# Optimization experiments

Hardware: AMD Instinct MI355X
Metric: run time of the kernel (lower is better)

## Reference

```python
import jax, jax.numpy as jnp
import numpy as np

N, L, D = 8192, 50, 64          # batch nodes, history length, embed_dim
NUM_ITEMS, NUM_ATTRS, NUM_FAM = 50000, 100000, 100000


def setup_inputs() -> dict:
    key = jax.random.key(0)
    ks = jax.random.split(key, 12)
    scale = 0.05
    return {
        "nodes": jax.random.randint(ks[0], (N,), 0, NUM_ITEMS),
        "history_va": jax.random.randint(ks[1], (N, L), 0, NUM_ATTRS),
        "history_af": jax.random.randint(ks[2], (N, L), 0, NUM_FAM),
        "v2e_w": jax.random.normal(ks[3], (NUM_ITEMS, D), jnp.float32) * scale,
        "a2e_w": jax.random.normal(ks[4], (NUM_ATTRS, D), jnp.float32) * scale,
        "f2e_w": jax.random.normal(ks[5], (NUM_FAM, D), jnp.float32) * scale,
        "W1": jax.random.normal(ks[6], (3 * D, D), jnp.float32) * scale,
        "b1": jnp.zeros((D,), jnp.float32),
        "W2": jax.random.normal(ks[7], (D, D), jnp.float32) * scale,
        "b2": jnp.zeros((D,), jnp.float32),
        "w3": jax.random.normal(ks[8], (D, 1), jnp.float32) * scale,
        "b3": jnp.zeros((1,), jnp.float32),
    }


def reference(nodes, history_va, history_af, v2e_w, a2e_w, f2e_w,
              W1, b1, W2, b2, w3, b3):
    # Batched form of the per-node loop (va=True branch).
    e_va = a2e_w[history_va]                       # [N, L, D] gathered attr embeds
    e_af = f2e_w[history_af]                       # [N, L, D] gathered famous embeds
    va_rep = v2e_w[nodes]                          # [N, D]    target item embed
    rep = jnp.broadcast_to(va_rep[:, None, :], e_va.shape)
    x = jnp.concatenate([e_va, rep, e_af], axis=-1)  # [N, L, 3D]
    h = jax.nn.relu(x @ W1 + b1)                   # [N, L, D]
    h = jax.nn.relu(h @ W2 + b2)                   # [N, L, D]
    scores = (h @ w3 + b3)[..., 0]                 # [N, L]
    att = jax.nn.softmax(scores, axis=1)           # softmax over history dim
    # e_va.T @ att per node  ==  weighted sum over history
    return jnp.einsum("nld,nl->nd", e_va, att)     # [N, D]
```

## Files before the change

kernel.cpp:

```cpp
#include <hip/hip_runtime.h>
#include <hip/hip_bf16.h>

typedef __bf16    bf16x8 __attribute__((ext_vector_type(8)));
typedef __bf16    bf16x4 __attribute__((ext_vector_type(4)));
typedef _Float16  f16x8  __attribute__((ext_vector_type(8)));
typedef _Float16  f16x4  __attribute__((ext_vector_type(4)));
typedef float     f32x4  __attribute__((ext_vector_type(4)));

#define HL 50
#define DD 64


__global__ __launch_bounds__(256, 4) void prep_all_kernel(
    const int*   __restrict__ nodes,
    const float* __restrict__ v2e,
    const float* __restrict__ W1,
    const float* __restrict__ b1,
    const float* __restrict__ W2,
    const float* __restrict__ b2,
    const float* __restrict__ w3,
    _Float16* __restrict__ ba16,
    _Float16* __restrict__ wf, float* __restrict__ wsc,
    int N, int GB)
{
    __shared__ __align__(16) _Float16 es[64 * 72];
    const int tid  = threadIdx.x;
    const int w    = tid >> 6, lane = tid & 63;
    const int lq   = lane & 15, quad = lane >> 4;
    const int bid  = blockIdx.x;

    if (bid < GB) {
        const int col = w * 16 + lq;
        const int n0 = bid * 64;
        #pragma unroll
        for (int i = 0; i < 4; ++i) {
            int t = i * 256 + tid;
            int row = t >> 4, q = t & 15;
            int gn = n0 + row; if (gn >= N) gn = N - 1;
            int idx = nodes[gn];
            float4 v = *(const float4*)(v2e + (size_t)idx * DD + q * 4);
            f16x4 pk = {(_Float16)v.x, (_Float16)v.y, (_Float16)v.z, (_Float16)v.w};
            *(f16x4*)&es[row * 72 + q * 4] = pk;
        }
        f16x8 bfr[2];
        #pragma unroll
        for (int t = 0; t < 2; ++t)
            #pragma unroll
            for (int j = 0; j < 8; ++j)
                bfr[t][j] = (_Float16)W1[(64 + t * 32 + quad * 8 + j) * DD + col];
        const float b1c = b1[col];
        __syncthreads();

        f32x4 acc[4];
        #pragma unroll
        for (int mt = 0; mt < 4; ++mt) acc[mt] = (f32x4){0.f, 0.f, 0.f, 0.f};
        #pragma unroll
        for (int t = 0; t < 2; ++t)
            #pragma unroll
            for (int mt = 0; mt < 4; ++mt) {
                f16x8 a = *(const f16x8*)&es[(mt * 16 + lq) * 72 + t * 32 + quad * 8];
                acc[mt] = __builtin_amdgcn_mfma_f32_16x16x32_f16(a, bfr[t], acc[mt], 0, 0, 0);
            }
        #pragma unroll
        for (int mt = 0; mt < 4; ++mt)
            #pragma unroll
            for (int r = 0; r < 4; ++r) {
                int gn = n0 + mt * 16 + quad * 4 + r;
                if (gn < N) ba16[(size_t)gn * DD + col] = (_Float16)(acc[mt][r] + b1c);
            }
    } else {
        const int ln = tid & 63, c0 = tid >> 6;
        #pragma unroll
        for (int h = 0; h < 6; ++h) {
            int c = c0 + 4 * h;
            int part = c >> 3, cc = c & 7;
            int ct = cc >> 1, t = cc & 1;
            const float* S = (part == 2) ? W2 : W1;
            int koff = (part == 1) ? 128 : 0;
            _Float16* d = wf + ((size_t)c * 64 + ln) * 8;
            #pragma unroll
            for (int j = 0; j < 8; ++j)
                d[j] = (_Float16)S[(koff + t * 32 + (ln >> 4) * 8 + j) * DD
                                   + ct * 16 + (ln & 15)];
        }
        if (tid < 64) { wsc[tid] = w3[tid]; wsc[64 + tid] = b2[tid]; }
    }
}

__global__ __launch_bounds__(256, 2) void va_main_kernel(
    const int*      __restrict__ hva,
    const int*      __restrict__ haf,
    const float*    __restrict__ a2e,
    const float*    __restrict__ f2e,
    const _Float16* __restrict__ ba16,
    const _Float16* __restrict__ wf,
    const float*    __restrict__ wsc,
    float*          __restrict__ out, int Ntot)
{
    __shared__ __align__(16) _Float16 hs[4][64 * 72];
    const int tid  = threadIdx.x;
    const int w    = tid >> 6;
    const int lane = tid & 63;
    const int lq   = lane & 15;
    const int quad = lane >> 4;
    const int node = blockIdx.x * 4 + w;
    if (node >= Ntot) return;
    _Float16* ws_ = hs[w];

    const int* hb = hva + node * HL;
    const int* fb = haf + node * HL;
    const int lclamp = (lane < HL) ? lane : 0;
    const int iv  = hb[lclamp];
    const int ifv = fb[lclamp];

    float4 ra[4][2][2];
    #pragma unroll
    for (int mt = 0; mt < 4; ++mt) {
        const int row = mt * 16 + lq;
        const int ia  = __shfl(iv, row);
        #pragma unroll
        for (int t = 0; t < 2; ++t) {
            const float* p = a2e + (size_t)ia * DD + t * 32 + quad * 8;
            ra[mt][t][0] = *(const float4*)p;
            ra[mt][t][1] = *(const float4*)(p + 4);
        }
    }
    f16x8 xa[4][2];
    #pragma unroll
    for (int mt = 0; mt < 4; ++mt)
        #pragma unroll
        for (int t = 0; t < 2; ++t) {
            float4 v0 = ra[mt][t][0], v1 = ra[mt][t][1];
            xa[mt][t] = (f16x8){(_Float16)v0.x, (_Float16)v0.y, (_Float16)v0.z, (_Float16)v0.w,
                                (_Float16)v1.x, (_Float16)v1.y, (_Float16)v1.z, (_Float16)v1.w};
        }

    float4 rf[4][2][2];
    #pragma unroll
    for (int mt = 0; mt < 4; ++mt) {
        const int row = mt * 16 + lq;
        const int ifm = __shfl(ifv, row);
        #pragma unroll
        for (int t = 0; t < 2; ++t) {
            const float* p = f2e + (size_t)ifm * DD + t * 32 + quad * 8;
            rf[mt][t][0] = *(const float4*)p;
            rf[mt][t][1] = *(const float4*)(p + 4);
        }
    }

    f32x4 acc[4][4];
    #pragma unroll
    for (int ct = 0; ct < 4; ++ct) {
        const float bav = (float)ba16[(size_t)node * DD + ct * 16 + lq];
        #pragma unroll
        for (int mt = 0; mt < 4; ++mt)
            acc[mt][ct] = (f32x4){bav, bav, bav, bav};
    }
    #pragma unroll
    for (int ct = 0; ct < 4; ++ct)
        #pragma unroll
        for (int t = 0; t < 2; ++t) {
            f16x8 bfr = *(const f16x8*)(wf + ((size_t)(ct * 2 + t) * 64 + lane) * 8);
            #pragma unroll
            for (int mt = 0; mt < 4; ++mt)
                acc[mt][ct] = __builtin_amdgcn_mfma_f32_16x16x32_f16(xa[mt][t], bfr, acc[mt][ct], 0, 0, 0);
        }
    f16x8 xf[4][2];
    #pragma unroll
    for (int mt = 0; mt < 4; ++mt)
        #pragma unroll
        for (int t = 0; t < 2; ++t) {
            float4 v0 = rf[mt][t][0], v1 = rf[mt][t][1];
            xf[mt][t] = (f16x8){(_Float16)v0.x, (_Float16)v0.y, (_Float16)v0.z, (_Float16)v0.w,
                                (_Float16)v1.x, (_Float16)v1.y, (_Float16)v1.z, (_Float16)v1.w};
        }
    #pragma unroll
    for (int ct = 0; ct < 4; ++ct)
        #pragma unroll
        for (int t = 0; t < 2; ++t) {
            f16x8 bfr = *(const f16x8*)(wf + ((size_t)(8 + ct * 2 + t) * 64 + lane) * 8);
            #pragma unroll
            for (int mt = 0; mt < 4; ++mt)
                acc[mt][ct] = __builtin_amdgcn_mfma_f32_16x16x32_f16(xf[mt][t], bfr, acc[mt][ct], 0, 0, 0);
        }

    #pragma unroll
    for (int mt = 0; mt < 4; ++mt)
        #pragma unroll
        for (int ct = 0; ct < 4; ++ct)
            #pragma unroll
            for (int r = 0; r < 4; ++r) {
                const int row = mt * 16 + quad * 4 + r;
                float hv = (row < HL) ? fmaxf(acc[mt][ct][r], 0.f) : 0.f;
                ws_[row * 72 + ct * 16 + lq] = (_Float16)hv;
            }

    f16x8 h1f[4][2];
    #pragma unroll
    for (int mt = 0; mt < 4; ++mt)
        #pragma unroll
        for (int t = 0; t < 2; ++t)
            h1f[mt][t] = *(const f16x8*)&ws_[(mt * 16 + lq) * 72 + t * 32 + quad * 8];

    float sc[4][4];
    #pragma unroll
    for (int mt = 0; mt < 4; ++mt)
        #pragma unroll
        for (int r = 0; r < 4; ++r) sc[mt][r] = 0.f;

    #pragma unroll
    for (int ct = 0; ct < 4; ++ct) {
        const float b2c = wsc[64 + ct * 16 + lq];
        const float w3c = wsc[ct * 16 + lq];
        f16x8 bfr[2];
        #pragma unroll
        for (int t = 0; t < 2; ++t)
            bfr[t] = *(const f16x8*)(wf + ((size_t)(16 + ct * 2 + t) * 64 + lane) * 8);
        #pragma unroll
        for (int mt = 0; mt < 4; ++mt) {
            f32x4 a2 = {b2c, b2c, b2c, b2c};
            #pragma unroll
            for (int t = 0; t < 2; ++t)
                a2 = __builtin_amdgcn_mfma_f32_16x16x32_f16(h1f[mt][t], bfr[t], a2, 0, 0, 0);
            #pragma unroll
            for (int r = 0; r < 4; ++r)
                sc[mt][r] = fmaf(fmaxf(a2[r], 0.f), w3c, sc[mt][r]);
        }
    }

    #pragma unroll
    for (int mt = 0; mt < 4; ++mt)
        #pragma unroll
        for (int r = 0; r < 4; ++r)
            #pragma unroll
            for (int m = 1; m < 16; m <<= 1)
                sc[mt][r] += __shfl_xor(sc[mt][r], m);

    #pragma unroll
    for (int r = 0; r < 4; ++r)
        if (48 + quad * 4 + r >= HL) sc[3][r] = -3.0e38f;

    float mx = sc[0][0];
    #pragma unroll
    for (int mt = 0; mt < 4; ++mt)
        #pragma unroll
        for (int r = 0; r < 4; ++r) mx = fmaxf(mx, sc[mt][r]);
    mx = fmaxf(mx, __shfl_xor(mx, 16));
    mx = fmaxf(mx, __shfl_xor(mx, 32));

    float sm = 0.f;
    #pragma unroll
    for (int mt = 0; mt < 4; ++mt)
        #pragma unroll
        for (int r = 0; r < 4; ++r) {
            sc[mt][r] = __expf(sc[mt][r] - mx);
            sm += sc[mt][r];
        }
    sm += __shfl_xor(sm, 16);
    sm += __shfl_xor(sm, 32);
    const float inv = 1.f / sm;

    float oa[4] = {0.f, 0.f, 0.f, 0.f};
    #pragma unroll
    for (int l = 0; l < HL; ++l) {
        const int   srcl = ((l >> 2) & 3) << 4;
        const float av   = __shfl(sc[l >> 4][l & 3], srcl);
        const int   idx  = __builtin_amdgcn_readlane(iv, l);
        oa[l & 3] = fmaf(av, a2e[(size_t)idx * DD + lane], oa[l & 3]);
    }
    out[(size_t)node * DD + lane] = ((oa[0] + oa[1]) + (oa[2] + oa[3])) * inv;
}

#define FMR  112
#define FMT  7
#define FXSS 136

__global__ __launch_bounds__(256) void fb_prep_kernel(
    const float* __restrict__ W1, const float* __restrict__ W2,
    const float* __restrict__ w3, const float* __restrict__ b1,
    const float* __restrict__ b2,
    __bf16* __restrict__ wf, float* __restrict__ wsc)
{
    const int tid  = threadIdx.x;
    const int quad = tid >> 6;
    const int col  = tid & 63;
    __bf16* dst = wf + tid * 64;
    #pragma unroll
    for (int t = 0; t < 4; ++t)
        #pragma unroll
        for (int j = 0; j < 8; ++j) {
            int keff = t * 32 + quad * 8 + j;
            int krow = (keff < 64) ? keff : keff + 64;
            dst[t * 8 + j] = (__bf16)W1[krow * 64 + col];
        }
    #pragma unroll
    for (int t = 0; t < 2; ++t)
        #pragma unroll
        for (int j = 0; j < 8; ++j) {
            dst[32 + t * 8 + j] = (__bf16)W1[(64 + t * 32 + quad * 8 + j) * 64 + col];
            dst[48 + t * 8 + j] = (__bf16)W2[(t * 32 + quad * 8 + j) * 64 + col];
        }
    if (tid < 64) {
        wsc[tid] = w3[tid]; wsc[64 + tid] = b1[tid]; wsc[128 + tid] = b2[tid];
    }
}

__global__ __launch_bounds__(256, 5) void fb_agg_kernel(
    const int* __restrict__ nodes, const int* __restrict__ hva,
    const int* __restrict__ haf, const float* __restrict__ v2e,
    const float* __restrict__ a2e, const float* __restrict__ f2e,
    const __bf16* __restrict__ wf, const float* __restrict__ wsc,
    float* __restrict__ out)
{
    __shared__ __bf16 xs[FMR * FXSS];
    __shared__ float  pbuf[4 * FMR];
    const int tid = threadIdx.x;
    const int w = tid >> 6, lane = tid & 63, lq = lane & 15, quad = lane >> 4;
    const int col = w * 16 + lq;
    const int n0 = blockIdx.x * 2;
    {
        const int* hb = hva + n0 * HL;
        const int* fb = haf + n0 * HL;
        #pragma unroll
        for (int i = 0; i < 13; ++i) {
            int t = i * 256 + tid;
            if (t < 2 * HL * 2 * 16) {
                int r = t >> 4, q = t & 15;
                bool va = (r < 2 * HL);
                int gr = va ? r : r - 2 * HL;
                int idx = va ? hb[gr] : fb[gr];
                const float* src = (va ? a2e : f2e) + (size_t)idx * DD + q * 4;
                float4 v = *(const float4*)src;
                bf16x4 pk = {(__bf16)v.x, (__bf16)v.y, (__bf16)v.z, (__bf16)v.w};
                *(bf16x4*)&xs[gr * FXSS + (va ? 0 : DD) + q * 4] = pk;
            }
        }
    }
    bf16x8 repf[2];
    #pragma unroll
    for (int t = 0; t < 2; ++t)
        #pragma unroll
        for (int j = 0; j < 8; ++j) repf[t][j] = (__bf16)0.f;
    if (lq < 2) {
        int nd = nodes[n0 + lq];
        const float* rp = v2e + (size_t)nd * DD;
        #pragma unroll
        for (int t = 0; t < 2; ++t) {
            float4 v0 = *(const float4*)(rp + t * 32 + quad * 8);
            float4 v1 = *(const float4*)(rp + t * 32 + quad * 8 + 4);
            repf[t] = (bf16x8){(__bf16)v0.x, (__bf16)v0.y, (__bf16)v0.z, (__bf16)v0.w,
                               (__bf16)v1.x, (__bf16)v1.y, (__bf16)v1.z, (__bf16)v1.w};
        }
    }
    const __bf16* fbp = wf + (size_t)(quad * 64 + col) * 64;
    bf16x8 b1f[4], b1u[2], b2f[2];
    #pragma unroll
    for (int t = 0; t < 4; ++t) b1f[t] = *(const bf16x8*)(fbp + t * 8);
    #pragma unroll
    for (int t = 0; t < 2; ++t) {
        b1u[t] = *(const bf16x8*)(fbp + 32 + t * 8);
        b2f[t] = *(const bf16x8*)(fbp + 48 + t * 8);
    }
    const float w3c = wsc[col];
    const float b1c = wsc[64 + col];
    const float b2c = wsc[128 + col];
    f32x4 rb = {0.f, 0.f, 0.f, 0.f};
    #pragma unroll
    for (int t = 0; t < 2; ++t)
        rb = __builtin_amdgcn_mfma_f32_16x16x32_bf16(repf[t], b1u[t], rb, 0, 0, 0);
    const float bias0 = __shfl(rb[0], lq) + b1c;
    const float bias1 = __shfl(rb[1], lq) + b1c;
    __syncthreads();
    f32x4 acc[FMT];
    #pragma unroll
    for (int mt = 0; mt < FMT; ++mt)
        #pragma unroll
        for (int r = 0; r < 4; ++r) {
            int gr = mt * 16 + quad * 4 + r;
            acc[mt][r] = (gr >= HL) ? bias1 : bias0;
        }
    #pragma unroll
    for (int t = 0; t < 4; ++t)
        #pragma unroll
        for (int mt = 0; mt < FMT; ++mt) {
            bf16x8 a = *(const bf16x8*)&xs[(mt * 16 + lq) * FXSS + t * 32 + quad * 8];
            acc[mt] = __builtin_amdgcn_mfma_f32_16x16x32_bf16(a, b1f[t], acc[mt], 0, 0, 0);
        }
    __syncthreads();
    #pragma unroll
    for (int mt = 0; mt < FMT; ++mt)
        #pragma unroll
        for (int r = 0; r < 4; ++r) {
            int gr = mt * 16 + quad * 4 + r;
            xs[gr * FXSS + DD + col] = (__bf16)fmaxf(acc[mt][r], 0.f);
        }
    __syncthreads();
    f32x4 a2[FMT];
    #pragma unroll
    for (int mt = 0; mt < FMT; ++mt) a2[mt] = (f32x4){b2c, b2c, b2c, b2c};
    #pragma unroll
    for (int t = 0; t < 2; ++t)
        #pragma unroll
        for (int mt = 0; mt < FMT; ++mt) {
            bf16x8 a = *(const bf16x8*)&xs[(mt * 16 + lq) * FXSS + DD + t * 32 + quad * 8];
            a2[mt] = __builtin_amdgcn_mfma_f32_16x16x32_bf16(a, b2f[t], a2[mt], 0, 0, 0);
        }
    #pragma unroll
    for (int mt = 0; mt < FMT; ++mt) {
        float p0 = fmaxf(a2[mt][0], 0.f) * w3c;
        float p1 = fmaxf(a2[mt][1], 0.f) * w3c;
        float p2 = fmaxf(a2[mt][2], 0.f) * w3c;
        float p3 = fmaxf(a2[mt][3], 0.f) * w3c;
        #pragma unroll
        for (int m = 1; m < 16; m <<= 1) {
            p0 += __shfl_xor(p0, m); p1 += __shfl_xor(p1, m);
            p2 += __shfl_xor(p2, m); p3 += __shfl_xor(p3, m);
        }
        if (lq == 0) {
            int rowb = mt * 16 + quad * 4;
            pbuf[w * FMR + rowb + 0] = p0; pbuf[w * FMR + rowb + 1] = p1;
            pbuf[w * FMR + rowb + 2] = p2; pbuf[w * FMR + rowb + 3] = p3;
        }
    }
    __syncthreads();
    const int n = w & 1, lh = w >> 1;
    float att;
    {
        float s = -3.0e38f;
        if (lane < HL) {
            int gr = n * HL + lane;
            s = pbuf[gr] + pbuf[FMR + gr] + pbuf[2 * FMR + gr] + pbuf[3 * FMR + gr];
        }
        float mx = s;
        #pragma unroll
        for (int m = 1; m < 64; m <<= 1) mx = fmaxf(mx, __shfl_xor(mx, m));
        float e = (lane < HL) ? __expf(s - mx) : 0.f;
        float sm = e;
        #pragma unroll
        for (int m = 1; m < 64; m <<= 1) sm += __shfl_xor(sm, m);
        att = e / sm;
    }
    {
        float o = 0.f;
        const int lb = lh * 25;
        #pragma unroll
        for (int i = 0; i < 25; ++i) {
            int l = lb + i;
            float av = __shfl(att, l);
            o = fmaf(av, (float)xs[(n * HL + l) * FXSS + lane], o);
        }
        float* op = (float*)&xs[(100 + w) * FXSS + DD];
        op[lane] = o;
    }
    __syncthreads();
    if (w < 2) {
        const float* p0 = (const float*)&xs[(100 + w) * FXSS + DD];
        const float* p1 = (const float*)&xs[(100 + w + 2) * FXSS + DD];
        out[(size_t)(n0 + w) * DD + lane] = p0[lane] + p1[lane];
    }
}

extern "C" void kernel_launch(void* const* d_in, const int* in_sizes, int n_in,
                              void* d_out, int out_size, void* d_ws, size_t ws_size,
                              hipStream_t stream) {
    const int*   nodes = (const int*)d_in[0];
    const int*   hva   = (const int*)d_in[1];
    const int*   haf   = (const int*)d_in[2];
    const float* v2e   = (const float*)d_in[3];
    const float* a2e   = (const float*)d_in[4];
    const float* f2e   = (const float*)d_in[5];
    const float* W1    = (const float*)d_in[6];
    const float* b1    = (const float*)d_in[7];
    const float* W2    = (const float*)d_in[8];
    const float* b2    = (const float*)d_in[9];
    const float* w3    = (const float*)d_in[10];
    float* out = (float*)d_out;

    const int N  = in_sizes[0];

    size_t offBA = 0;
    size_t offWF = (offBA + (size_t)N * DD * 2 + 255) & ~(size_t)255;
    size_t offSC = offWF + 24 * 64 * 8 * 2;
    size_t need  = offSC + 128 * 4;

    if (ws_size >= need) {
        _Float16* ba  = (_Float16*)((char*)d_ws + offBA);
        _Float16* wfr = (_Float16*)((char*)d_ws + offWF);
        float*    wsc = (float*)((char*)d_ws + offSC);

        const int GB = (N + 63) / 64;
        prep_all_kernel<<<GB + 1, 256, 0, stream>>>(
            nodes, v2e, W1, b1, W2, b2, w3, ba, wfr, wsc, N, GB);
        va_main_kernel<<<(N + 3) / 4, 256, 0, stream>>>(
            hva, haf, a2e, f2e, ba, wfr, wsc, out, N);
    } else {
        __bf16* wf  = (__bf16*)d_ws;
        float*  wsc = (float*)((char*)d_ws + 256 * 64 * 2);
        fb_prep_kernel<<<1, 256, 0, stream>>>(W1, W2, w3, b1, b2, wf, wsc);
        fb_agg_kernel<<<N / 2, 256, 0, stream>>>(nodes, hva, haf, v2e, a2e, f2e,
                                                 wf, wsc, out);
    }
}
```

Measured before the change: 164.7 us.

## Pre-convert full attr/famous embedding tables to fp16 before gather

Adds a prep pass that converts the whole a2e and f2e tables (200k rows) to fp16 in workspace, and the main kernel then gathers fp16 rows, halving per-gather bytes and removing in-kernel conversions. The conversion reads about 51 MB and writes about 25 MB every call, while the main kernel only gathers about 2*8192*50 rows, roughly 210 MB of fp32 before. The final weighted sum now uses fp16-rounded embeddings, which lowers output precision.

```diff
diff --git a/kernel.cpp b/kernel.cpp
--- a/kernel.cpp
+++ b/kernel.cpp
@@ -14,14 +14,17 @@
 __global__ __launch_bounds__(256, 4) void prep_all_kernel(
     const int*   __restrict__ nodes,
     const float* __restrict__ v2e,
+    const float* __restrict__ a2e,
+    const float* __restrict__ f2e,
     const float* __restrict__ W1,
     const float* __restrict__ b1,
     const float* __restrict__ W2,
     const float* __restrict__ b2,
     const float* __restrict__ w3,
+    _Float16* __restrict__ A16, _Float16* __restrict__ F16,
     _Float16* __restrict__ ba16,
     _Float16* __restrict__ wf, float* __restrict__ wsc,
-    int N, int GB)
+    int nA, int nF, int N, int GC, int GB)
 {
     __shared__ __align__(16) _Float16 es[64 * 72];
     const int tid  = threadIdx.x;
@@ -29,9 +32,29 @@
     const int lq   = lane & 15, quad = lane >> 4;
     const int bid  = blockIdx.x;
 
-    if (bid < GB) {
+    if (bid < GC) {
+        const size_t total = (size_t)(nA + nF) * 16;
+        for (size_t c = (size_t)bid * 256 + tid; c < total;
+             c += (size_t)GC * 256) {
+            const size_t row = c >> 4;
+            const int    seg = (int)(c & 15);
+            const float* s;
+            _Float16*    d;
+            if (row < (size_t)nA) {
+                s = a2e + row * DD + seg * 4;
+                d = A16 + row * DD + seg * 4;
+            } else {
+                const size_t r2 = row - (size_t)nA;
+                s = f2e + r2 * DD + seg * 4;
+                d = F16 + r2 * DD + seg * 4;
+            }
+            float4 v = *(const float4*)s;
+            f16x4 pk = {(_Float16)v.x, (_Float16)v.y, (_Float16)v.z, (_Float16)v.w};
+            *(f16x4*)d = pk;
+        }
+    } else if (bid < GC + GB) {
         const int col = w * 16 + lq;
-        const int n0 = bid * 64;
+        const int n0 = (bid - GC) * 64;
         #pragma unroll
         for (int i = 0; i < 4; ++i) {
             int t = i * 256 + tid;
@@ -90,8 +113,8 @@
 __global__ __launch_bounds__(256, 2) void va_main_kernel(
     const int*      __restrict__ hva,
     const int*      __restrict__ haf,
-    const float*    __restrict__ a2e,
-    const float*    __restrict__ f2e,
+    const _Float16* __restrict__ A16,
+    const _Float16* __restrict__ F16,
     const _Float16* __restrict__ ba16,
     const _Float16* __restrict__ wf,
     const float*    __restrict__ wsc,
@@ -113,38 +136,16 @@
     const int iv  = hb[lclamp];
     const int ifv = fb[lclamp];
 
-    float4 ra[4][2][2];
+    f16x8 xa[4][2], xf[4][2];
     #pragma unroll
     for (int mt = 0; mt < 4; ++mt) {
         const int row = mt * 16 + lq;
-        const int ia  = __shfl(iv, row);
+        const int ia  = __shfl(iv,  row);
+        const int ifm = __shfl(ifv, row);
         #pragma unroll
         for (int t = 0; t < 2; ++t) {
-            const float* p = a2e + (size_t)ia * DD + t * 32 + quad * 8;
-            ra[mt][t][0] = *(const float4*)p;
-            ra[mt][t][1] = *(const float4*)(p + 4);
-        }
-    }
-    f16x8 xa[4][2];
-    #pragma unroll
-    for (int mt = 0; mt < 4; ++mt)
-        #pragma unroll
-        for (int t = 0; t < 2; ++t) {
-            float4 v0 = ra[mt][t][0], v1 = ra[mt][t][1];
-            xa[mt][t] = (f16x8){(_Float16)v0.x, (_Float16)v0.y, (_Float16)v0.z, (_Float16)v0.w,
-                                (_Float16)v1.x, (_Float16)v1.y, (_Float16)v1.z, (_Float16)v1.w};
-        }
-
-    float4 rf[4][2][2];
-    #pragma unroll
-    for (int mt = 0; mt < 4; ++mt) {
-        const int row = mt * 16 + lq;
-        const int ifm = __shfl(ifv, row);
-        #pragma unroll
-        for (int t = 0; t < 2; ++t) {
-            const float* p = f2e + (size_t)ifm * DD + t * 32 + quad * 8;
-            rf[mt][t][0] = *(const float4*)p;
-            rf[mt][t][1] = *(const float4*)(p + 4);
+            xa[mt][t] = *(const f16x8*)(A16 + (size_t)ia  * DD + t * 32 + quad * 8);
+            xf[mt][t] = *(const f16x8*)(F16 + (size_t)ifm * DD + t * 32 + quad * 8);
         }
     }
 
@@ -164,15 +165,6 @@
             #pragma unroll
             for (int mt = 0; mt < 4; ++mt)
                 acc[mt][ct] = __builtin_amdgcn_mfma_f32_16x16x32_f16(xa[mt][t], bfr, acc[mt][ct], 0, 0, 0);
-        }
-    f16x8 xf[4][2];
-    #pragma unroll
-    for (int mt = 0; mt < 4; ++mt)
-        #pragma unroll
-        for (int t = 0; t < 2; ++t) {
-            float4 v0 = rf[mt][t][0], v1 = rf[mt][t][1];
-            xf[mt][t] = (f16x8){(_Float16)v0.x, (_Float16)v0.y, (_Float16)v0.z, (_Float16)v0.w,
-                                (_Float16)v1.x, (_Float16)v1.y, (_Float16)v1.z, (_Float16)v1.w};
         }
     #pragma unroll
     for (int ct = 0; ct < 4; ++ct)
@@ -266,7 +258,7 @@
         const int   srcl = ((l >> 2) & 3) << 4;
         const float av   = __shfl(sc[l >> 4][l & 3], srcl);
         const int   idx  = __builtin_amdgcn_readlane(iv, l);
-        oa[l & 3] = fmaf(av, a2e[(size_t)idx * DD + lane], oa[l & 3]);
+        oa[l & 3] = fmaf(av, (float)A16[(size_t)idx * DD + lane], oa[l & 3]);
     }
     out[(size_t)node * DD + lane] = ((oa[0] + oa[1]) + (oa[2] + oa[3])) * inv;
 }
@@ -477,22 +469,30 @@
     float* out = (float*)d_out;
 
     const int N  = in_sizes[0];
-
-    size_t offBA = 0;
+    const int nA = in_sizes[4] / DD;
+    const int nF = in_sizes[5] / DD;
+
+    size_t offA  = 0;
+    size_t offF  = (offA + (size_t)nA * DD * 2 + 255) & ~(size_t)255;
+    size_t offBA = (offF + (size_t)nF * DD * 2 + 255) & ~(size_t)255;
     size_t offWF = (offBA + (size_t)N * DD * 2 + 255) & ~(size_t)255;
     size_t offSC = offWF + 24 * 64 * 8 * 2;
     size_t need  = offSC + 128 * 4;
 
     if (ws_size >= need) {
+        _Float16* A16 = (_Float16*)((char*)d_ws + offA);
+        _Float16* F16 = (_Float16*)((char*)d_ws + offF);
         _Float16* ba  = (_Float16*)((char*)d_ws + offBA);
         _Float16* wfr = (_Float16*)((char*)d_ws + offWF);
         float*    wsc = (float*)((char*)d_ws + offSC);
 
+        const int GC = 2048;
         const int GB = (N + 63) / 64;
-        prep_all_kernel<<<GB + 1, 256, 0, stream>>>(
-            nodes, v2e, W1, b1, W2, b2, w3, ba, wfr, wsc, N, GB);
+        prep_all_kernel<<<GC + GB + 1, 256, 0, stream>>>(
+            nodes, v2e, a2e, f2e, W1, b1, W2, b2, w3,
+            A16, F16, ba, wfr, wsc, nA, nF, N, GC, GB);
         va_main_kernel<<<(N + 3) / 4, 256, 0, stream>>>(
-            hva, haf, a2e, f2e, ba, wfr, wsc, out, N);
+            hva, haf, A16, F16, ba, wfr, wsc, out, N);
     } else {
         __bf16* wf  = (__bf16*)d_ws;
         float*  wsc = (float*)((char*)d_ws + 256 * 64 * 2);
```

New measurement: 159.2 us. -3.4%, faster.
